# Kernel optimization log

Hardware: AMD Instinct MI355X
Metric: run time of the kernel (lower is better)

Reference implementation:

```python
import jax, jax.numpy as jnp
import numpy as np

TEMPERATURE = 0.5


def setup_inputs() -> dict:
    key = jax.random.key(0)
    k1, k2 = jax.random.split(key)
    N, D = 4096, 256
    z_i = jax.random.normal(k1, (N, D), dtype=jnp.float32)
    z_j = jax.random.normal(k2, (N, D), dtype=jnp.float32)
    return {"z_i": z_i, "z_j": z_j}


def reference(z_i, z_j):
    N = z_i.shape[0]
    z = jnp.concatenate([z_i, z_j], axis=0)            # (2N, D)
    sim = (z @ z.T) / TEMPERATURE                       # (2N, 2N)
    # mask self-similarity on the diagonal
    diag = jnp.eye(2 * N, dtype=bool)
    sim = jnp.where(diag, -jnp.inf, sim)
    # positive pair labels: i <-> i+N
    labels = jnp.concatenate([jnp.arange(N, 2 * N), jnp.arange(0, N)])
    logp = jax.nn.log_softmax(sim, axis=-1)             # (2N, 2N)
    loss = -jnp.mean(jnp.take_along_axis(logp, labels[:, None], axis=-1))
    return loss
```

## Files before the change

### kernel.cpp

```cpp
#include <hip/hip_runtime.h>
#include <hip/hip_bf16.h>


typedef __bf16 bf16x8 __attribute__((ext_vector_type(8)));
typedef __bf16 bf16x4 __attribute__((ext_vector_type(4)));
typedef float  f32x16 __attribute__((ext_vector_type(16)));

#define NPAIR 4096
#define NROW  8192
#define DIM   256
#define STRIPS 16
#define RBLK  16384
#define SQSCALE 1.6986437f
#define LN2F    0.6931471805599453f
#define M2      176.0f

#define EXP2F(x) __builtin_amdgcn_exp2f(x)

__global__ __launch_bounds__(256) void k_convert(const float* __restrict__ zi,
                                                 const float* __restrict__ zj,
                                                 __bf16* __restrict__ Zf,
                                                 float* __restrict__ pos,
                                                 float* __restrict__ out) {
    const int w = threadIdx.x >> 6, lane = threadIdx.x & 63;
    const int r = blockIdx.x * 4 + w;
    if (blockIdx.x == 0 && threadIdx.x == 0) out[0] = 0.0f;
    const float4 vi = *(const float4*)(zi + r * DIM + lane * 4);
    const float4 vj = *(const float4*)(zj + r * DIM + lane * 4);
    bf16x4 bi, bj;
    bi[0] = (__bf16)(vi.x * SQSCALE); bi[1] = (__bf16)(vi.y * SQSCALE);
    bi[2] = (__bf16)(vi.z * SQSCALE); bi[3] = (__bf16)(vi.w * SQSCALE);
    bj[0] = (__bf16)(vj.x * SQSCALE); bj[1] = (__bf16)(vj.y * SQSCALE);
    bj[2] = (__bf16)(vj.z * SQSCALE); bj[3] = (__bf16)(vj.w * SQSCALE);
    const int t = lane >> 2, h = (lane >> 1) & 1, inner = (lane & 1) * 8;
    char* Zb = (char*)Zf;
    *(bf16x4*)(Zb + (size_t)(r >> 5) * RBLK + t * 1024 + h * 512 + (r & 31) * 16 + inner) = bi;
    const int r2 = r + NPAIR;
    *(bf16x4*)(Zb + (size_t)(r2 >> 5) * RBLK + t * 1024 + h * 512 + (r2 & 31) * 16 + inner) = bj;
    float d = vi.x * vj.x + vi.y * vj.y + vi.z * vj.z + vi.w * vj.w;
    #pragma unroll
    for (int m = 32; m >= 1; m >>= 1) d += __shfl_xor(d, m);
    if (lane == 0) pos[r] = 2.0f * d;
}

__global__ __launch_bounds__(256, 2) void k_lse(const __bf16* __restrict__ Zf,
                                                float* __restrict__ Lpart) {
    const int bx    = blockIdx.x;
    const int rb    = bx & 31;
    const int strip = bx >> 5;
    const int tid   = threadIdx.x;
    const int w     = tid >> 6;
    const int lane  = tid & 63, lm = lane & 31, half = lane >> 5;
    const int laneoff = half * 512 + lm * 16;
    const int R0 = rb * 8 + w * 2, R1 = R0 + 1;

    __shared__ __align__(16) char smem[65536];
    const char* Zb = (const char*)Zf;

    const char* g0 = Zb + (size_t)R0 * RBLK + laneoff;
    const char* g1 = Zb + (size_t)R1 * RBLK + laneoff;
    #define LOADB(i) \
        bf16x8 B0_##i = *(const bf16x8*)(g0 + (i) * 1024); \
        bf16x8 B1_##i = *(const bf16x8*)(g1 + (i) * 1024);
    LOADB(0)  LOADB(1)  LOADB(2)  LOADB(3)
    LOADB(4)  LOADB(5)  LOADB(6)  LOADB(7)
    LOADB(8)  LOADB(9)  LOADB(10) LOADB(11)
    LOADB(12) LOADB(13) LOADB(14) LOADB(15)
    #undef LOADB

    const char* Acol = Zb + (size_t)strip * 16 * RBLK;

    #define STAGE(bufsel, phidx) do {                                              \
        const char* _s = Acol + (size_t)(phidx) * RBLK + tid * 16;                 \
        char*       _d = smem + (bufsel) * 16384 + tid * 16;                       \
        _Pragma("unroll")                                                          \
        for (int _q = 0; _q < 4; _q++)                                             \
            __builtin_amdgcn_global_load_lds(                                      \
                (const __attribute__((address_space(1))) unsigned int*)(_s + _q * 4096), \
                (__attribute__((address_space(3))) unsigned int*)(_d + _q * 4096), \
                16, 0, 0);                                                         \
    } while (0)

    float l0 = 0.0f, l1 = 0.0f;

    #define MSTEP(i) {                                                             \
        bf16x8 a_ = *(const bf16x8*)(Ab + (i) * 1024);                             \
        acc0 = __builtin_amdgcn_mfma_f32_32x32x16_bf16(a_, B0_##i, acc0, 0, 0, 0); \
        acc1 = __builtin_amdgcn_mfma_f32_32x32x16_bf16(a_, B1_##i, acc1, 0, 0, 0); \
    }

    #define PHASE_BODY(PH, WAITSTR, DO_STAGE) do {                                 \
        asm volatile("s_waitcnt vmcnt(" WAITSTR ")" ::: "memory");                 \
        __builtin_amdgcn_s_barrier();                                              \
        asm volatile("" ::: "memory");                                             \
        if (DO_STAGE) STAGE(((PH) + 3) & 3, (PH) + 3);                             \
        const char* Ab = smem + ((PH) & 3) * 16384 + laneoff;                      \
        f32x16 acc0 = (f32x16)(0.0f);                                              \
        f32x16 acc1 = (f32x16)(0.0f);                                              \
        __builtin_amdgcn_s_setprio(1);                                             \
        MSTEP(0)  MSTEP(1)  MSTEP(2)  MSTEP(3)                                     \
        MSTEP(4)  MSTEP(5)  MSTEP(6)  MSTEP(7)                                     \
        MSTEP(8)  MSTEP(9)  MSTEP(10) MSTEP(11)                                    \
        MSTEP(12) MSTEP(13) MSTEP(14) MSTEP(15)                                    \
        __builtin_amdgcn_s_setprio(0);                                             \
        const int cb = strip * 16 + (PH);                                          \
        if (cb == R0) {            \
            _Pragma("unroll")                                                      \
            for (int rg = 0; rg < 16; rg++) {                                      \
                const int cl = (rg & 3) + 8 * (rg >> 2) + 4 * half;                \
                acc0[rg] = (cl == lm) ? -1e30f : acc0[rg];                         \
            }                                                                      \
        }                                                                          \
        if (cb == R1) {                                                            \
            _Pragma("unroll")                                                      \
            for (int rg = 0; rg < 16; rg++) {                                      \
                const int cl = (rg & 3) + 8 * (rg >> 2) + 4 * half;                \
                acc1[rg] = (cl == lm) ? -1e30f : acc1[rg];                         \
            }                                                                      \
        }                                                                          \
        float p0 = 0.0f, p1 = 0.0f, q0 = 0.0f, q1 = 0.0f;                          \
        _Pragma("unroll")                                                          \
        for (int rg = 0; rg < 16; rg += 2) {                                       \
            p0 += EXP2F(acc0[rg]     - M2);                                        \
            p1 += EXP2F(acc0[rg + 1] - M2);                                        \
            q0 += EXP2F(acc1[rg]     - M2);                                        \
            q1 += EXP2F(acc1[rg + 1] - M2);                                        \
        }                                                                          \
        l0 += p0 + p1;                                                             \
        l1 += q0 + q1;                                                             \
    } while (0)

    STAGE(0, 0);
    STAGE(1, 1);
    STAGE(2, 2);

    for (int ph = 0; ph < 14; ph++) {
        PHASE_BODY(ph, "8", ph < 13);
    }
    PHASE_BODY(14, "4", 0);
    PHASE_BODY(15, "0", 0);

    #undef PHASE_BODY
    #undef MSTEP
    #undef STAGE

    l0 += __shfl_xor(l0, 32);
    l1 += __shfl_xor(l1, 32);
    if (half == 0) {
        Lpart[strip * NROW + R0 * 32 + lm] = l0;
        Lpart[strip * NROW + R1 * 32 + lm] = l1;
    }
}

__global__ __launch_bounds__(256) void k_final(const float* __restrict__ Lpart,
                                               const float* __restrict__ pos,
                                               float* __restrict__ out) {
    __shared__ float red[256];
    const int t = threadIdx.x;
    const int r = blockIdx.x * 256 + t;
    float l = 0.0f;
    #pragma unroll
    for (int s = 0; s < STRIPS; s++) l += Lpart[s * NROW + r];
    const float lse = (M2 + __builtin_log2f(l)) * LN2F;
    red[t] = lse - pos[r & (NPAIR - 1)];
    __syncthreads();
    for (int ofs = 128; ofs > 0; ofs >>= 1) {
        if (t < ofs) red[t] += red[t + ofs];
        __syncthreads();
    }
    if (t == 0) atomicAdd(out, red[0] / (float)NROW);
}

extern "C" void kernel_launch(void* const* d_in, const int* in_sizes, int n_in,
                              void* d_out, int out_size, void* d_ws, size_t ws_size,
                              hipStream_t stream) {
    const float* zi = (const float*)d_in[0];
    const float* zj = (const float*)d_in[1];
    __bf16* Zf   = (__bf16*)d_ws;
    float* pos   = (float*)((char*)d_ws + (size_t)NROW * DIM * 2);
    float* Lpart = pos + NPAIR;

    k_convert<<<NPAIR / 4, 256, 0, stream>>>(zi, zj, Zf, pos, (float*)d_out);
    k_lse<<<32 * STRIPS, 256, 0, stream>>>(Zf, Lpart);
    k_final<<<NROW / 256, 256, 0, stream>>>(Lpart, pos, (float*)d_out);
}
```

Before: 95.55 us.

## Software-pipeline exp epilogue of previous tile under current tile's MFMAs

Double-buffers the accumulator tiles across phases, so the exp2 reduction of the previous phase's scores is interleaved with the MFMA chain of the current phase. Scheduling group barriers pin the MFMA, LDS read and VALU interleaving. The aim is to hide the transcendental and VALU epilogue behind matrix-core work. In exchange it doubles accumulator register pressure, which may hurt occupancy, and adds a drain epilogue after the last phase. The initial -1e30 fill makes the first phase's exp contribution effectively zero.

```diff
diff --git a/kernel.cpp b/kernel.cpp
--- a/kernel.cpp
+++ b/kernel.cpp
@@ -83,66 +83,89 @@
 
     float l0 = 0.0f, l1 = 0.0f;
 
-    #define MSTEP(i) {                                                             \
+    f32x16 accA0 = (f32x16)(-1e30f), accA1 = (f32x16)(-1e30f);
+    f32x16 accB0 = (f32x16)(-1e30f), accB1 = (f32x16)(-1e30f);
+
+    #define MSTEP(i, ...) {                                                        \
         bf16x8 a_ = *(const bf16x8*)(Ab + (i) * 1024);                             \
-        acc0 = __builtin_amdgcn_mfma_f32_32x32x16_bf16(a_, B0_##i, acc0, 0, 0, 0); \
-        acc1 = __builtin_amdgcn_mfma_f32_32x32x16_bf16(a_, B1_##i, acc1, 0, 0, 0); \
-    }
-
-    #define PHASE_BODY(PH, WAITSTR, DO_STAGE) do {                                 \
+        WA0 = __builtin_amdgcn_mfma_f32_32x32x16_bf16(a_, B0_##i, WA0, 0, 0, 0);   \
+        WA1 = __builtin_amdgcn_mfma_f32_32x32x16_bf16(a_, B1_##i, WA1, 0, 0, 0);   \
+        __VA_ARGS__                                                                \
+        __builtin_amdgcn_sched_group_barrier(0x100, 1, 0);                         \
+        __builtin_amdgcn_sched_group_barrier(0x008, 2, 0);                         \
+        __builtin_amdgcn_sched_group_barrier(0x002, 6, 0);                         \
+    }
+
+    #define PHASE_BODY(PH, PA0, PA1, PR0, PR1, WAITSTR, DO_STAGE) do {             \
         asm volatile("s_waitcnt vmcnt(" WAITSTR ")" ::: "memory");                 \
         __builtin_amdgcn_s_barrier();                                              \
         asm volatile("" ::: "memory");                                             \
         if (DO_STAGE) STAGE(((PH) + 3) & 3, (PH) + 3);                             \
         const char* Ab = smem + ((PH) & 3) * 16384 + laneoff;                      \
-        f32x16 acc0 = (f32x16)(0.0f);                                              \
-        f32x16 acc1 = (f32x16)(0.0f);                                              \
+        f32x16 &WA0 = PA0, &WA1 = PA1;                                             \
+        const f32x16 &RA0 = PR0, &RA1 = PR1;                                       \
+        WA0 = (f32x16)(0.0f);                                                      \
+        WA1 = (f32x16)(0.0f);                                                      \
+        float e0 = 0.0f, e1 = 0.0f, e2 = 0.0f, e3 = 0.0f;                          \
         __builtin_amdgcn_s_setprio(1);                                             \
-        MSTEP(0)  MSTEP(1)  MSTEP(2)  MSTEP(3)                                     \
-        MSTEP(4)  MSTEP(5)  MSTEP(6)  MSTEP(7)                                     \
-        MSTEP(8)  MSTEP(9)  MSTEP(10) MSTEP(11)                                    \
-        MSTEP(12) MSTEP(13) MSTEP(14) MSTEP(15)                                    \
+        MSTEP(0,  e0 += EXP2F(RA0[0]  - M2); e1 += EXP2F(RA0[1]  - M2);)           \
+        MSTEP(1,  e0 += EXP2F(RA0[2]  - M2); e1 += EXP2F(RA0[3]  - M2);)           \
+        MSTEP(2,  e0 += EXP2F(RA0[4]  - M2); e1 += EXP2F(RA0[5]  - M2);)           \
+        MSTEP(3,  e0 += EXP2F(RA0[6]  - M2); e1 += EXP2F(RA0[7]  - M2);)           \
+        MSTEP(4,  e0 += EXP2F(RA0[8]  - M2); e1 += EXP2F(RA0[9]  - M2);)           \
+        MSTEP(5,  e0 += EXP2F(RA0[10] - M2); e1 += EXP2F(RA0[11] - M2);)           \
+        MSTEP(6,  e0 += EXP2F(RA0[12] - M2); e1 += EXP2F(RA0[13] - M2);)           \
+        MSTEP(7,  e0 += EXP2F(RA0[14] - M2); e1 += EXP2F(RA0[15] - M2);)           \
+        MSTEP(8,  e2 += EXP2F(RA1[0]  - M2); e3 += EXP2F(RA1[1]  - M2);)           \
+        MSTEP(9,  e2 += EXP2F(RA1[2]  - M2); e3 += EXP2F(RA1[3]  - M2);)           \
+        MSTEP(10, e2 += EXP2F(RA1[4]  - M2); e3 += EXP2F(RA1[5]  - M2);)           \
+        MSTEP(11, e2 += EXP2F(RA1[6]  - M2); e3 += EXP2F(RA1[7]  - M2);)           \
+        MSTEP(12, e2 += EXP2F(RA1[8]  - M2); e3 += EXP2F(RA1[9]  - M2);)           \
+        MSTEP(13, e2 += EXP2F(RA1[10] - M2); e3 += EXP2F(RA1[11] - M2);)           \
+        MSTEP(14, e2 += EXP2F(RA1[12] - M2); e3 += EXP2F(RA1[13] - M2);)           \
+        MSTEP(15, e2 += EXP2F(RA1[14] - M2); e3 += EXP2F(RA1[15] - M2);)           \
         __builtin_amdgcn_s_setprio(0);                                             \
         const int cb = strip * 16 + (PH);                                          \
-        if (cb == R0) {            \
+        if (cb == R0) {             \
             _Pragma("unroll")                                                      \
             for (int rg = 0; rg < 16; rg++) {                                      \
                 const int cl = (rg & 3) + 8 * (rg >> 2) + 4 * half;                \
-                acc0[rg] = (cl == lm) ? -1e30f : acc0[rg];                         \
+                WA0[rg] = (cl == lm) ? -1e30f : WA0[rg];                           \
             }                                                                      \
         }                                                                          \
         if (cb == R1) {                                                            \
             _Pragma("unroll")                                                      \
             for (int rg = 0; rg < 16; rg++) {                                      \
                 const int cl = (rg & 3) + 8 * (rg >> 2) + 4 * half;                \
-                acc1[rg] = (cl == lm) ? -1e30f : acc1[rg];                         \
+                WA1[rg] = (cl == lm) ? -1e30f : WA1[rg];                           \
             }                                                                      \
         }                                                                          \
-        float p0 = 0.0f, p1 = 0.0f, q0 = 0.0f, q1 = 0.0f;                          \
-        _Pragma("unroll")                                                          \
-        for (int rg = 0; rg < 16; rg += 2) {                                       \
-            p0 += EXP2F(acc0[rg]     - M2);                                        \
-            p1 += EXP2F(acc0[rg + 1] - M2);                                        \
-            q0 += EXP2F(acc1[rg]     - M2);                                        \
-            q1 += EXP2F(acc1[rg + 1] - M2);                                        \
-        }                                                                          \
-        l0 += p0 + p1;                                                             \
-        l1 += q0 + q1;                                                             \
+        l0 += e0 + e1;                                                             \
+        l1 += e2 + e3;                                                             \
     } while (0)
 
     STAGE(0, 0);
     STAGE(1, 1);
     STAGE(2, 2);
 
-    for (int ph = 0; ph < 14; ph++) {
-        PHASE_BODY(ph, "8", ph < 13);
-    }
-    PHASE_BODY(14, "4", 0);
-    PHASE_BODY(15, "0", 0);
+    for (int ph = 0; ph < 12; ph += 2) {
+        PHASE_BODY(ph,     accA0, accA1, accB0, accB1, "8", 1);
+        PHASE_BODY(ph + 1, accB0, accB1, accA0, accA1, "8", 1);
+    }
+    PHASE_BODY(12, accA0, accA1, accB0, accB1, "8", 1);
+    PHASE_BODY(13, accB0, accB1, accA0, accA1, "8", 0);
+    PHASE_BODY(14, accA0, accA1, accB0, accB1, "4", 0);
+    PHASE_BODY(15, accB0, accB1, accA0, accA1, "0", 0);
 
     #undef PHASE_BODY
     #undef MSTEP
     #undef STAGE
+
+    #pragma unroll
+    for (int rg = 0; rg < 16; rg++) {
+        l0 += EXP2F(accB0[rg] - M2);
+        l1 += EXP2F(accB1[rg] - M2);
+    }
 
     l0 += __shfl_xor(l0, 32);
     l1 += __shfl_xor(l1, 32);
```

After: 99.07 us. 1.04x slower.
